# Optimization experiments

Hardware: AMD Instinct MI355X
Metric: run time of the kernel (lower is better)

## Reference

```python
import jax, jax.numpy as jnp
import numpy as np

N_EMBD = 1024
N_HEAD = 64

def setup_inputs() -> dict:
    key = jax.random.key(0)
    ks = jax.random.split(key, 7)
    B, T = 4, 4096
    x = jax.random.normal(ks[0], (B, T, N_EMBD), dtype=jnp.float32)
    # causal mask: True above the diagonal (masked positions)
    mask = jnp.triu(jnp.ones((T, T), dtype=bool), k=1)
    s = 1.0 / np.sqrt(N_EMBD)
    Wq = jax.random.normal(ks[1], (N_EMBD, N_HEAD), dtype=jnp.float32) * s
    bq = jnp.zeros((N_HEAD,), dtype=jnp.float32)
    Wk = jax.random.normal(ks[2], (N_EMBD, N_HEAD), dtype=jnp.float32) * s
    bk = jnp.zeros((N_HEAD,), dtype=jnp.float32)
    Wv = jax.random.normal(ks[3], (N_EMBD, N_HEAD), dtype=jnp.float32) * s
    bv = jnp.zeros((N_HEAD,), dtype=jnp.float32)
    return {"x": x, "mask": mask, "Wq": Wq, "bq": bq, "Wk": Wk, "bk": bk, "Wv": Wv, "bv": bv}

def reference(x, mask, Wq, bq, Wk, bk, Wv, bv):
    # x: [B,T,C], mask: [T,T] bool (True = masked)
    q = x @ Wq + bq            # [B,T,H]
    k = x @ Wk + bk            # [B,T,H]
    v = x @ Wv + bv            # [B,T,H]
    scale = 1.0 / jnp.sqrt(jnp.asarray(q.shape[-1], dtype=q.dtype))
    att = jnp.einsum('bth,bsh->bts', q, k) * scale   # [B,T,T]
    att = jnp.where(mask[None, :, :], -jnp.inf, att)
    att = jax.nn.softmax(att, axis=-1)
    # dropout omitted (eval mode / deterministic reference)
    return jnp.einsum('bts,bsh->bth', att, v)        # [B,T,H]
```

## Files before the change

### kernel.cpp

```cpp
#include <hip/hip_runtime.h>
#include <hip/hip_bf16.h>

#define BB 4
#define TT 4096
#define CC 1024
#define HH 64

#define QSCALE 0.18033688011112042f
#define FIXMAX2 23.083120654223414f

typedef __attribute__((ext_vector_type(8))) short short8;
typedef __attribute__((ext_vector_type(8))) ushort ushortx8;
typedef __attribute__((ext_vector_type(4))) float floatx4;

__device__ __forceinline__ ushort f2bf(float f) {
    union { float f; unsigned u; } a; a.f = f;
    const unsigned u = a.u;
    return (ushort)((u + 0x7fffu + ((u >> 16) & 1u)) >> 16);
}
__device__ __forceinline__ float bf2f(ushort h) {
    union { unsigned u; float f; } a; a.u = ((unsigned)h) << 16; return a.f;
}

__global__ __launch_bounds__(256)
void wtrans_kernel(const float* __restrict__ Wq, const float* __restrict__ Wk,
                   const float* __restrict__ Wv, ushort* __restrict__ wTf)
{
    const int tid = threadIdx.x;
    const int kc = blockIdx.x;
    #pragma unroll
    for (int it = 0; it < 6; ++it) {
        const int s = it * 256 + tid;
        const int lane = s & 63;
        const int t = s >> 6;
        const int j = t % 3;
        const int qv = t / 3;
        const int wv = qv & 3, ks = qv >> 2;
        const int r = wv * 48 + j * 16 + (lane & 15);
        const int mat = r >> 6, n = r & 63;
        const int k0 = kc * 64 + ks * 32 + (lane >> 4) * 8;
        const float* W = (mat == 0) ? Wq : (mat == 1) ? Wk : Wv;
        ushortx8 o;
        #pragma unroll
        for (int e = 0; e < 8; ++e)
            o[e] = f2bf(W[(size_t)(k0 + e) * 64 + n]);
        *(ushortx8*)(wTf + ((size_t)(kc * 24 + t) * 64 + lane) * 8) = o;
    }
}

__global__ __launch_bounds__(256)
void qkv_mfma_kernel(const float* __restrict__ x, const ushort* __restrict__ wTf,
                     const float* __restrict__ bq, const float* __restrict__ bk,
                     const float* __restrict__ bv,
                     ushort* __restrict__ q, ushort* __restrict__ k,
                     ushort* __restrict__ vT)
{
    __shared__ ushort xs[2][32 * 72];

    const int tid = threadIdx.x, w = tid >> 6, lane = tid & 63;
    const int m = lane & 15, quad = lane >> 4;
    const int row0 = blockIdx.x * 32;

    floatx4 acc[2][3];
    #pragma unroll
    for (int mi = 0; mi < 2; ++mi)
        #pragma unroll
        for (int j = 0; j < 3; ++j) acc[mi][j] = (floatx4){0.f, 0.f, 0.f, 0.f};

    const ushort* gb = wTf + (size_t)w * 1536 + lane * 8;

    const int xr = tid >> 3, xseg = tid & 7;
    const float* gx = x + (size_t)(row0 + xr) * CC + xseg * 8;

    short8 bcur[3][2], bnxt[3][2];

    #pragma unroll
    for (int j = 0; j < 3; ++j)
        #pragma unroll
        for (int ks_ = 0; ks_ < 2; ++ks_)
            bcur[j][ks_] = *(const short8*)(gb + ks_ * 6144 + j * 512);
    {
        const float4 xa = *(const float4*)(gx);
        const float4 xb = *(const float4*)(gx + 4);
        ushortx8 p;
        p[0] = f2bf(xa.x); p[1] = f2bf(xa.y); p[2] = f2bf(xa.z); p[3] = f2bf(xa.w);
        p[4] = f2bf(xb.x); p[5] = f2bf(xb.y); p[6] = f2bf(xb.z); p[7] = f2bf(xb.w);
        *(ushortx8*)(&xs[0][xr * 72 + xseg * 8]) = p;
    }
    __syncthreads();

    for (int kc = 0; kc < 16; ++kc) {
        const int cur = kc & 1;
        float4 na, nb;
        if (kc < 15) {
            const int k0n = (kc + 1) * 64;
            na = *(const float4*)(gx + k0n);
            nb = *(const float4*)(gx + k0n + 4);
            const ushort* gn = gb + (size_t)(kc + 1) * 12288;
            #pragma unroll
            for (int j = 0; j < 3; ++j)
                #pragma unroll
                for (int ks_ = 0; ks_ < 2; ++ks_)
                    bnxt[j][ks_] = *(const short8*)(gn + ks_ * 6144 + j * 512);
        }
        const ushort* xb_ = xs[cur];
        #pragma unroll
        for (int mi = 0; mi < 2; ++mi) {
            const short8 a0 = *(const short8*)(xb_ + (mi * 16 + m) * 72 + quad * 8);
            const short8 a1 = *(const short8*)(xb_ + (mi * 16 + m) * 72 + 32 + quad * 8);
            #pragma unroll
            for (int j = 0; j < 3; ++j) {
                acc[mi][j] = __builtin_amdgcn_mfma_f32_16x16x32_bf16(a0, bcur[j][0], acc[mi][j], 0, 0, 0);
                acc[mi][j] = __builtin_amdgcn_mfma_f32_16x16x32_bf16(a1, bcur[j][1], acc[mi][j], 0, 0, 0);
            }
        }
        if (kc < 15) {
            ushortx8 p;
            p[0] = f2bf(na.x); p[1] = f2bf(na.y); p[2] = f2bf(na.z); p[3] = f2bf(na.w);
            p[4] = f2bf(nb.x); p[5] = f2bf(nb.y); p[6] = f2bf(nb.z); p[7] = f2bf(nb.w);
            *(ushortx8*)(&xs[cur ^ 1][xr * 72 + xseg * 8]) = p;
            #pragma unroll
            for (int j = 0; j < 3; ++j) {
                bcur[j][0] = bnxt[j][0];
                bcur[j][1] = bnxt[j][1];
            }
        }
        __syncthreads();
    }

    const int b_ = row0 >> 12, tb = row0 & (TT - 1);
    #pragma unroll
    for (int j = 0; j < 3; ++j) {
        const int nt = w * 3 + j;
        const int mat = nt >> 2;
        const int c = (nt & 3) * 16 + m;
        const float bias = (mat == 0) ? bq[c] : (mat == 1) ? bk[c] : bv[c];
        #pragma unroll
        for (int mi = 0; mi < 2; ++mi) {
            const int gr0 = row0 + mi * 16 + quad * 4;
            if (mat == 0) {
                #pragma unroll
                for (int r = 0; r < 4; ++r)
                    q[(size_t)(gr0 + r) * HH + c] = f2bf((acc[mi][j][r] + bias) * QSCALE);
            } else if (mat == 1) {
                #pragma unroll
                for (int r = 0; r < 4; ++r)
                    k[(size_t)(gr0 + r) * HH + c] = f2bf(acc[mi][j][r] + bias);
            } else {
                ushort4 pv;
                pv.x = f2bf(acc[mi][j][0] + bias); pv.y = f2bf(acc[mi][j][1] + bias);
                pv.z = f2bf(acc[mi][j][2] + bias); pv.w = f2bf(acc[mi][j][3] + bias);
                const int t0 = tb + mi * 16 + quad * 4;
                *(ushort4*)(vT + ((size_t)b_ * HH + c) * TT + t0) = pv;
            }
        }
    }
}

__global__ __launch_bounds__(256)
void attn_mfma_kernel(const ushort* __restrict__ q, const ushort* __restrict__ k,
                      const ushort* __restrict__ vT,
                      float* __restrict__ partL, ushort* __restrict__ partO)
{
    __shared__ ushort ks[64 * 72];
    __shared__ ushort vs[64 * 72];
    __shared__ ushort ps[4][16 * 72];

    const int tid = threadIdx.x, w = tid >> 6, lane = tid & 63;
    const int m = lane & 15, quad = lane >> 4;
    const int xcd = blockIdx.x & 7;
    const int pos = blockIdx.x >> 3;
    const int b = xcd >> 1;
    const int idx = (pos << 1) | (xcd & 1);
    const int split = idx & 7;
    const int tile = 63 - (idx >> 3);
    const int job = (b << 6) | tile;
    const int pid = job * 8 + split;
    const int i0 = tile * 64;
    const int nch = tile + 1;
    const int lo = (nch * split) >> 3, hi = (nch * (split + 1)) >> 3;

    const size_t qrow = ((size_t)b * TT + i0 + w * 16 + m) * HH;
    const uint4 aq0u = *(const uint4*)(q + qrow + quad * 8);
    const uint4 aq1u = *(const uint4*)(q + qrow + 32 + quad * 8);
    const short8 aq0 = *(const short8*)&aq0u;
    const short8 aq1 = *(const short8*)&aq1u;

    float lrow[4] = {0.f, 0.f, 0.f, 0.f};
    floatx4 oacc[4];
    #pragma unroll
    for (int nt = 0; nt < 4; ++nt) oacc[nt] = (floatx4){0.f, 0.f, 0.f, 0.f};

    const int iq0 = i0 + w * 16;
    for (int ch = lo; ch < hi; ++ch) {
        const int s0 = ch * 64;
        __syncthreads();
        const size_t kb = ((size_t)b * TT + s0) * HH;
        #pragma unroll
        for (int it = 0; it < 2; ++it) {
            const int t2 = it * 256 + tid;
            const int r = t2 >> 3, seg = t2 & 7;
            *(uint4*)(ks + r * 72 + seg * 8) = *(const uint4*)(k + kb + (size_t)r * HH + seg * 8);
            *(uint4*)(vs + r * 72 + seg * 8) = *(const uint4*)(vT + ((size_t)b * HH + r) * TT + s0 + seg * 8);
        }
        __syncthreads();

        floatx4 sc[4];
        __builtin_amdgcn_s_setprio(1);
        #pragma unroll
        for (int nt = 0; nt < 4; ++nt) {
            const short8 b0 = *(const short8*)(ks + (nt * 16 + m) * 72 + quad * 8);
            const short8 b1 = *(const short8*)(ks + (nt * 16 + m) * 72 + 32 + quad * 8);
            floatx4 s_ = (floatx4){0.f, 0.f, 0.f, 0.f};
            s_ = __builtin_amdgcn_mfma_f32_16x16x32_bf16(aq0, b0, s_, 0, 0, 0);
            s_ = __builtin_amdgcn_mfma_f32_16x16x32_bf16(aq1, b1, s_, 0, 0, 0);
            sc[nt] = s_;
        }
        __builtin_amdgcn_s_setprio(0);

        const bool need_mask = (s0 + 63 > iq0);
        #pragma unroll
        for (int r = 0; r < 4; ++r) {
            float t0 = sc[0][r] - FIXMAX2;
            float t1 = sc[1][r] - FIXMAX2;
            float t2 = sc[2][r] - FIXMAX2;
            float t3 = sc[3][r] - FIXMAX2;
            if (need_mask) {
                const int dlim = iq0 + quad * 4 + r - s0 - m;
                if (0  > dlim) t0 = -1e30f;
                if (16 > dlim) t1 = -1e30f;
                if (32 > dlim) t2 = -1e30f;
                if (48 > dlim) t3 = -1e30f;
            }
            const float p0 = __builtin_amdgcn_exp2f(t0);
            const float p1 = __builtin_amdgcn_exp2f(t1);
            const float p2 = __builtin_amdgcn_exp2f(t2);
            const float p3 = __builtin_amdgcn_exp2f(t3);
            lrow[r] += (p0 + p1) + (p2 + p3);
            ushort* pr = ps[w] + (quad * 4 + r) * 72;
            pr[m]      = f2bf(p0);
            pr[16 + m] = f2bf(p1);
            pr[32 + m] = f2bf(p2);
            pr[48 + m] = f2bf(p3);
        }

        __builtin_amdgcn_s_setprio(1);
        #pragma unroll
        for (int ks_ = 0; ks_ < 2; ++ks_) {
            const short8 ap = *(const short8*)(ps[w] + m * 72 + ks_ * 32 + quad * 8);
            #pragma unroll
            for (int nt = 0; nt < 4; ++nt) {
                const short8 bv_ = *(const short8*)(vs + (nt * 16 + m) * 72 + ks_ * 32 + quad * 8);
                oacc[nt] = __builtin_amdgcn_mfma_f32_16x16x32_bf16(ap, bv_, oacc[nt], 0, 0, 0);
            }
        }
        __builtin_amdgcn_s_setprio(0);
    }

    #pragma unroll
    for (int r = 0; r < 4; ++r) {
        float s = lrow[r];
        s += __shfl_xor(s, 1); s += __shfl_xor(s, 2);
        s += __shfl_xor(s, 4); s += __shfl_xor(s, 8);
        lrow[r] = s;
    }
    if (m == 0) {
        #pragma unroll
        for (int r = 0; r < 4; ++r)
            partL[(size_t)pid * 64 + w * 16 + quad * 4 + r] = lrow[r];
    }
    ushort* po = partO + ((size_t)pid * 64 + w * 16) * 64;
    #pragma unroll
    for (int r = 0; r < 4; ++r) {
        const int row = quad * 4 + r;
        #pragma unroll
        for (int nt = 0; nt < 4; ++nt)
            po[row * 64 + nt * 16 + m] = f2bf(oacc[nt][r]);
    }
}

__global__ __launch_bounds__(256)
void attn_combine_kernel(const float* __restrict__ partL,
                         const ushort* __restrict__ partO, float* __restrict__ out)
{
    const int job = blockIdx.x;
    const int tid = threadIdx.x;
    const int row = tid >> 2, dq = tid & 3;

    float L = 0.f;
    #pragma unroll
    for (int s = 0; s < 8; ++s) L += partL[(size_t)(job * 8 + s) * 64 + row];
    const float inv = 1.f / L;

    float o[16];
    #pragma unroll
    for (int i = 0; i < 16; ++i) o[i] = 0.f;
    #pragma unroll
    for (int s = 0; s < 8; ++s) {
        const ushort* po = partO + (((size_t)(job * 8 + s) * 64 + row) * 64 + dq * 16);
        #pragma unroll
        for (int i2 = 0; i2 < 2; ++i2) {
            const ushort4 pa = *(const ushort4*)(po + i2 * 8);
            const ushort4 pb = *(const ushort4*)(po + i2 * 8 + 4);
            o[i2*8+0] += bf2f(pa.x); o[i2*8+1] += bf2f(pa.y);
            o[i2*8+2] += bf2f(pa.z); o[i2*8+3] += bf2f(pa.w);
            o[i2*8+4] += bf2f(pb.x); o[i2*8+5] += bf2f(pb.y);
            o[i2*8+6] += bf2f(pb.z); o[i2*8+7] += bf2f(pb.w);
        }
    }
    float4* dst = (float4*)(out + ((size_t)job * 64 + row) * 64 + dq * 16);
    #pragma unroll
    for (int i = 0; i < 4; ++i) {
        float4 v; v.x = o[i*4]*inv; v.y = o[i*4+1]*inv; v.z = o[i*4+2]*inv; v.w = o[i*4+3]*inv;
        dst[i] = v;
    }
}

extern "C" void kernel_launch(void* const* d_in, const int* in_sizes, int n_in,
                              void* d_out, int out_size, void* d_ws, size_t ws_size,
                              hipStream_t stream) {
    (void)in_sizes; (void)n_in; (void)out_size; (void)ws_size;
    const float* x  = (const float*)d_in[0];
    const float* Wq = (const float*)d_in[2];
    const float* bq = (const float*)d_in[3];
    const float* Wk = (const float*)d_in[4];
    const float* bk = (const float*)d_in[5];
    const float* Wv = (const float*)d_in[6];
    const float* bv = (const float*)d_in[7];
    float* out = (float*)d_out;

    char* ws = (char*)d_ws;
    ushort* wTf   = (ushort*)ws;
    ushort* qb    = (ushort*)(ws + 393216);
    ushort* kb    = qb + (size_t)BB * TT * HH;
    ushort* vTb   = kb + (size_t)BB * TT * HH;
    float*  partL = (float*) (ws + 6684672);
    ushort* partO = (ushort*)(ws + 7208960);

    wtrans_kernel   <<<16, 256, 0, stream>>>(Wq, Wk, Wv, wTf);
    qkv_mfma_kernel <<<(BB * TT) / 32, 256, 0, stream>>>(x, wTf, bq, bk, bv, qb, kb, vTb);
    attn_mfma_kernel<<<BB * 64 * 8, 256, 0, stream>>>(qb, kb, vTb, partL, partO);
    attn_combine_kernel<<<BB * 64, 256, 0, stream>>>(partL, partO, out);
}
```

Before: 186.8 us.

## Split QKV projection K dimension across two wave groups with LDS reduction

Doubles the QKV projection block to 512 threads. The two halves of waves each handle half of the 1024-long reduction dimension over 8 chunks instead of 16, and their partial accumulators are summed through shared memory before the epilogue. The aim is to halve the serial K-loop latency per block and give the projection more parallelism to hide memory latency. The cost is extra LDS for the reduction buffer, an additional barrier, and larger blocks that may reduce how many blocks fit per CU.

```diff
diff --git a/kernel.cpp b/kernel.cpp
--- a/kernel.cpp
+++ b/kernel.cpp
@@ -48,16 +48,18 @@
     }
 }
 
-__global__ __launch_bounds__(256)
+__global__ __launch_bounds__(512)
 void qkv_mfma_kernel(const float* __restrict__ x, const ushort* __restrict__ wTf,
                      const float* __restrict__ bq, const float* __restrict__ bk,
                      const float* __restrict__ bv,
                      ushort* __restrict__ q, ushort* __restrict__ k,
                      ushort* __restrict__ vT)
 {
-    __shared__ ushort xs[2][32 * 72];
+    __shared__ ushort xs[2][2][32 * 72];
+    __shared__ float red[4 * 64 * 6 * 4];
 
     const int tid = threadIdx.x, w = tid >> 6, lane = tid & 63;
+    const int wn = w & 3, kh = w >> 2;
     const int m = lane & 15, quad = lane >> 4;
     const int row0 = blockIdx.x * 32;
 
@@ -67,10 +69,10 @@
         #pragma unroll
         for (int j = 0; j < 3; ++j) acc[mi][j] = (floatx4){0.f, 0.f, 0.f, 0.f};
 
-    const ushort* gb = wTf + (size_t)w * 1536 + lane * 8;
-
-    const int xr = tid >> 3, xseg = tid & 7;
-    const float* gx = x + (size_t)(row0 + xr) * CC + xseg * 8;
+    const ushort* gb = wTf + (size_t)wn * 1536 + lane * 8 + (size_t)kh * 8 * 12288;
+
+    const int xr = tid >> 4, khs = (tid >> 3) & 1, xseg = tid & 7;
+    const float* gx = x + (size_t)(row0 + xr) * CC + khs * 512 + xseg * 8;
 
     short8 bcur[3][2], bnxt[3][2];
 
@@ -85,25 +87,25 @@
         ushortx8 p;
         p[0] = f2bf(xa.x); p[1] = f2bf(xa.y); p[2] = f2bf(xa.z); p[3] = f2bf(xa.w);
         p[4] = f2bf(xb.x); p[5] = f2bf(xb.y); p[6] = f2bf(xb.z); p[7] = f2bf(xb.w);
-        *(ushortx8*)(&xs[0][xr * 72 + xseg * 8]) = p;
+        *(ushortx8*)(&xs[0][khs][xr * 72 + xseg * 8]) = p;
     }
     __syncthreads();
 
-    for (int kc = 0; kc < 16; ++kc) {
-        const int cur = kc & 1;
+    for (int c = 0; c < 8; ++c) {
+        const int cur = c & 1;
         float4 na, nb;
-        if (kc < 15) {
-            const int k0n = (kc + 1) * 64;
+        if (c < 7) {
+            const int k0n = (c + 1) * 64;
             na = *(const float4*)(gx + k0n);
             nb = *(const float4*)(gx + k0n + 4);
-            const ushort* gn = gb + (size_t)(kc + 1) * 12288;
+            const ushort* gn = gb + (size_t)(c + 1) * 12288;
             #pragma unroll
             for (int j = 0; j < 3; ++j)
                 #pragma unroll
                 for (int ks_ = 0; ks_ < 2; ++ks_)
                     bnxt[j][ks_] = *(const short8*)(gn + ks_ * 6144 + j * 512);
         }
-        const ushort* xb_ = xs[cur];
+        const ushort* xb_ = xs[cur][kh];
         #pragma unroll
         for (int mi = 0; mi < 2; ++mi) {
             const short8 a0 = *(const short8*)(xb_ + (mi * 16 + m) * 72 + quad * 8);
@@ -114,11 +116,11 @@
                 acc[mi][j] = __builtin_amdgcn_mfma_f32_16x16x32_bf16(a1, bcur[j][1], acc[mi][j], 0, 0, 0);
             }
         }
-        if (kc < 15) {
+        if (c < 7) {
             ushortx8 p;
             p[0] = f2bf(na.x); p[1] = f2bf(na.y); p[2] = f2bf(na.z); p[3] = f2bf(na.w);
             p[4] = f2bf(nb.x); p[5] = f2bf(nb.y); p[6] = f2bf(nb.z); p[7] = f2bf(nb.w);
-            *(ushortx8*)(&xs[cur ^ 1][xr * 72 + xseg * 8]) = p;
+            *(ushortx8*)(&xs[cur ^ 1][khs][xr * 72 + xseg * 8]) = p;
             #pragma unroll
             for (int j = 0; j < 3; ++j) {
                 bcur[j][0] = bnxt[j][0];
@@ -128,10 +130,25 @@
         __syncthreads();
     }
 
+    if (kh == 1) {
+        #pragma unroll
+        for (int mi = 0; mi < 2; ++mi)
+            #pragma unroll
+            for (int j = 0; j < 3; ++j)
+                *(floatx4*)(red + (((wn * 64 + lane) * 6 + mi * 3 + j) << 2)) = acc[mi][j];
+    }
+    __syncthreads();
+    if (kh == 1) return;
+    #pragma unroll
+    for (int mi = 0; mi < 2; ++mi)
+        #pragma unroll
+        for (int j = 0; j < 3; ++j)
+            acc[mi][j] += *(const floatx4*)(red + (((wn * 64 + lane) * 6 + mi * 3 + j) << 2));
+
     const int b_ = row0 >> 12, tb = row0 & (TT - 1);
     #pragma unroll
     for (int j = 0; j < 3; ++j) {
-        const int nt = w * 3 + j;
+        const int nt = wn * 3 + j;
         const int mat = nt >> 2;
         const int c = (nt & 3) * 16 + m;
         const float bias = (mat == 0) ? bq[c] : (mat == 1) ? bk[c] : bv[c];
@@ -338,7 +355,7 @@
     ushort* partO = (ushort*)(ws + 7208960);
 
     wtrans_kernel   <<<16, 256, 0, stream>>>(Wq, Wk, Wv, wTf);
-    qkv_mfma_kernel <<<(BB * TT) / 32, 256, 0, stream>>>(x, wTf, bq, bk, bv, qb, kb, vTb);
+    qkv_mfma_kernel <<<(BB * TT) / 32, 512, 0, stream>>>(x, wTf, bq, bk, bv, qb, kb, vTb);
     attn_mfma_kernel<<<BB * 64 * 8, 256, 0, stream>>>(qb, kb, vTb, partL, partO);
     attn_combine_kernel<<<BB * 64, 256, 0, stream>>>(partL, partO, out);
 }
```

After: 183.7 us. Within noise of the previous version (-1.7%).
